# Kernel optimization log

Hardware: AMD Instinct MI355X
Metric: run time of the kernel (lower is better)

The kernel has to match this reference:

```python
import jax, jax.numpy as jnp
import numpy as np

N_TOKENS = 2048
HIDDEN = 2880
N_HEADS = 64          # total query heads
N_KV = 8              # key/value heads
Q_MULT = N_HEADS // N_KV
HEAD_DIM = 64
SLIDING_WINDOW = 128  # layer_idx=0 -> sliding-window layer
SM_SCALE = 1.0 / np.sqrt(HEAD_DIM)
RMS_EPS = 1e-5
ROPE_BASE = 150000.0
ROPE_SCALING = 32.0
INIT_CTX = 4096
NTK_ALPHA = 1.0
NTK_BETA = 32.0


def _rope_tables(num_tokens):
    # YaRN NTK-by-parts inverse frequencies (static constants)
    freq = ROPE_BASE ** (np.arange(0, HEAD_DIM, 2, dtype=np.float64) / HEAD_DIM)
    concentration = 0.1 * np.log(ROPE_SCALING) + 1.0
    d_half = HEAD_DIM / 2
    low = d_half * np.log(INIT_CTX / (NTK_BETA * 2 * np.pi)) / np.log(ROPE_BASE)
    high = d_half * np.log(INIT_CTX / (NTK_ALPHA * 2 * np.pi)) / np.log(ROPE_BASE)
    interpolation = 1.0 / (ROPE_SCALING * freq)
    extrapolation = 1.0 / freq
    ramp = (np.arange(d_half) - low) / (high - low)
    m = 1.0 - np.clip(ramp, 0.0, 1.0)
    inv_freq = interpolation * (1.0 - m) + extrapolation * m
    t = np.arange(num_tokens, dtype=np.float64)
    freqs = np.outer(t, inv_freq)
    cos = jnp.asarray((np.cos(freqs) * concentration), dtype=jnp.float32)
    sin = jnp.asarray((np.sin(freqs) * concentration), dtype=jnp.float32)
    return cos, sin  # [num_tokens, HEAD_DIM//2]


def _apply_rotary(x, cos, sin):
    # x: [n, heads, HEAD_DIM]
    c = cos[:, None, :].astype(x.dtype)
    s = sin[:, None, :].astype(x.dtype)
    x1, x2 = jnp.split(x, 2, axis=-1)
    return jnp.concatenate([x1 * c - x2 * s, x2 * c + x1 * s], axis=-1)


def setup_inputs() -> dict:
    key = jax.random.key(0)
    ks = jax.random.split(key, 7)
    return {
        "x": jax.random.normal(ks[0], (N_TOKENS, HIDDEN), jnp.float32),
        "scale": jax.random.uniform(ks[1], (HIDDEN,), jnp.float32, 0.5, 1.5),
        "sink": jax.random.normal(ks[2], (N_HEADS,), jnp.float32),
        "w_qkv": jax.random.normal(ks[3], (HIDDEN, (N_HEADS + 2 * N_KV) * HEAD_DIM), jnp.float32) * 0.02,
        "b_qkv": jax.random.normal(ks[4], ((N_HEADS + 2 * N_KV) * HEAD_DIM,), jnp.float32) * 0.02,
        "w_o": jax.random.normal(ks[5], (N_HEADS * HEAD_DIM, HIDDEN), jnp.float32) * 0.02,
        "b_o": jax.random.normal(ks[6], (HIDDEN,), jnp.float32) * 0.02,
    }


def reference(x, scale, sink, w_qkv, b_qkv, w_o, b_o):
    n = x.shape[0]
    # RMSNorm (fp32)
    t = x.astype(jnp.float32)
    rms = jnp.sqrt(jnp.mean(t * t, axis=-1, keepdims=True) + RMS_EPS)
    t = (t / rms) * scale

    # QKV projection + split
    qkv = t @ w_qkv + b_qkv
    q_sz = N_HEADS * HEAD_DIM
    kv_sz = N_KV * HEAD_DIM
    q = qkv[:, :q_sz].reshape(n, N_HEADS, HEAD_DIM)
    k = qkv[:, q_sz:q_sz + kv_sz].reshape(n, N_KV, HEAD_DIM)
    v = qkv[:, q_sz + kv_sz:].reshape(n, N_KV, HEAD_DIM)

    # RoPE (YaRN)
    cos, sin = _rope_tables(n)
    q = _apply_rotary(q, cos, sin)
    k = _apply_rotary(k, cos, sin)

    # GQA layout: [n, N_KV, Q_MULT, HEAD_DIM]
    qg = q.reshape(n, N_KV, Q_MULT, HEAD_DIM)

    # scores: [N_KV, Q_MULT, n_q, n_kv]
    scores = jnp.einsum('nhgd,mhd->hgnm', qg, k) * SM_SCALE

    # causal + sliding-window mask
    q_pos = jnp.arange(n)[:, None]
    kv_pos = jnp.arange(n)[None, :]
    mask = jnp.where(kv_pos > q_pos, -jnp.inf, 0.0)
    mask = mask + jnp.where((SLIDING_WINDOW > 0) & (q_pos - kv_pos > SLIDING_WINDOW), -jnp.inf, 0.0)
    scores = scores + mask[None, None, :, :].astype(scores.dtype)

    # sink logit appended as extra softmax column, then dropped
    s_col = jnp.broadcast_to(sink.reshape(N_KV, Q_MULT, 1, 1), (N_KV, Q_MULT, n, 1))
    w = jax.nn.softmax(jnp.concatenate([scores, s_col], axis=-1), axis=-1)[..., :-1]

    attn = jnp.einsum('hgnm,mhd->nhgd', w, v).reshape(n, N_HEADS * HEAD_DIM)
    out = attn @ w_o + b_o
    return x + out


if __name__ == '__main__':
    inp = setup_inputs()
    y = reference(**inp)
    print(y.shape, y.dtype)
```

## Files before the change

### kernel.cpp

```cpp
#include <hip/hip_runtime.h>
#include <cstdint>
#include <cstddef>

#define HIDDEN   2880
#define QKV_N    5120
#define OPROJ_K  4096
#define NTOK     2048
#define WIN      128
#define SM_SCALE 0.125f

typedef _Float16 half8  __attribute__((ext_vector_type(8)));
typedef _Float16 half4v __attribute__((ext_vector_type(4)));
typedef float    f32x4  __attribute__((ext_vector_type(4)));

__device__ __forceinline__ void gload16(const void* g, void* l) {
  __builtin_amdgcn_global_load_lds((__attribute__((address_space(1))) void*)g,
                                   (__attribute__((address_space(3))) void*)l,
                                   16, 0, 0);
}

__device__ __forceinline__ _Float16 f2h(float f) { return (_Float16)f; }

#define NB_CQ  (160 * 90)
#define NB_CO  (92 * 128)
#define NB_ROPE 256

__device__ __forceinline__ void cast_transpose_body(const float* __restrict__ W,
                                                    _Float16* __restrict__ Wt,
                                                    int K, int N, int n0, int k0,
                                                    float* tile ) {
  int t = threadIdx.x;
  #pragma unroll
  for (int p = 0; p < 4; ++p) {
    int e = t + p * 256; int r = e >> 5, cc = e & 31;
    float vv = 0.f;
    if (n0 + cc < N) vv = W[(size_t)(k0 + r) * N + n0 + cc];
    tile[r * 33 + cc] = vv;
  }
  __syncthreads();
  {
    int r = t >> 3, c4 = (t & 7) * 4;
    half4v h;
    #pragma unroll
    for (int u = 0; u < 4; ++u) h[u] = (_Float16)tile[(c4 + u) * 33 + r];
    *(half4v*)&Wt[(size_t)(n0 + r) * K + k0 + c4] = h;
  }
}

__global__ __launch_bounds__(256) void prep_kernel(const float* __restrict__ x,
                                                   const float* __restrict__ scale,
                                                   const float* __restrict__ w_qkv,
                                                   const float* __restrict__ w_o,
                                                   _Float16* __restrict__ a_h,
                                                   _Float16* __restrict__ wtq,
                                                   _Float16* __restrict__ wto,
                                                   float2* __restrict__ tab) {
  __shared__ float smem[32 * 33];
  int b = blockIdx.x, t = threadIdx.x;
  if (b < NB_CQ) {
    cast_transpose_body(w_qkv, wtq, HIDDEN, QKV_N, (b % 160) * 32, (b / 160) * 32, smem);
    return;
  }
  b -= NB_CQ;
  if (b < NB_CO) {
    cast_transpose_body(w_o, wto, OPROJ_K, HIDDEN, (b % 92) * 32, (b / 92) * 32, smem);
    return;
  }
  b -= NB_CO;
  if (b < NTOK) {
    int row = b;
    const float4* xr = (const float4*)(x + (size_t)row * HIDDEN);
    const float4* sc = (const float4*)scale;
    float4 v0 = xr[t];
    float4 v1 = xr[t + 256];
    float4 v2 = (t < 208) ? xr[t + 512] : make_float4(0.f, 0.f, 0.f, 0.f);
    float ss = v0.x*v0.x + v0.y*v0.y + v0.z*v0.z + v0.w*v0.w
             + v1.x*v1.x + v1.y*v1.y + v1.z*v1.z + v1.w*v1.w
             + v2.x*v2.x + v2.y*v2.y + v2.z*v2.z + v2.w*v2.w;
    #pragma unroll
    for (int m = 1; m < 64; m <<= 1) ss += __shfl_xor(ss, m, 64);
    if ((t & 63) == 0) smem[t >> 6] = ss;
    __syncthreads();
    float inv = 1.0f / sqrtf((smem[0] + smem[1] + smem[2] + smem[3]) * (1.0f / HIDDEN) + 1e-5f);
    _Float16* orow = a_h + (size_t)row * HIDDEN;
    auto store4 = [&](int c4, const float4& v, const float4& s) {
      half4v h;
      h[0] = f2h(v.x * inv * s.x); h[1] = f2h(v.y * inv * s.y);
      h[2] = f2h(v.z * inv * s.z); h[3] = f2h(v.w * inv * s.w);
      *(half4v*)(orow + (size_t)c4 * 4) = h;
    };
    store4(t, v0, sc[t]);
    store4(t + 256, v1, sc[t + 256]);
    if (t < 208) store4(t + 512, v2, sc[t + 512]);
    return;
  }
  b -= NTOK;
  {
    int idx = b * 256 + t;
    int tok = idx >> 5, d = idx & 31;
    const double PI = 3.14159265358979323846;
    double i = (double)d;
    double lf = log(150000.0);
    double freq = exp(lf * (i / 32.0));
    double interp = 1.0 / (32.0 * freq);
    double extrap = 1.0 / freq;
    double low  = 32.0 * log(4096.0 / (32.0 * 2.0 * PI)) / lf;
    double high = 32.0 * log(4096.0 / (2.0 * PI)) / lf;
    double ramp = (i - low) / (high - low);
    double mm = 1.0 - fmin(fmax(ramp, 0.0), 1.0);
    double invf = interp * (1.0 - mm) + extrap * mm;
    double ang = (double)tok * invf;
    double conc = 0.1 * log(32.0) + 1.0;
    tab[idx] = make_float2((float)(cos(ang) * conc), (float)(sin(ang) * conc));
  }
}

template <int BM, bool QKV_MODE>
__global__ __launch_bounds__(256, 2) void gemm_kernel(const _Float16* __restrict__ A,
                                                      const _Float16* __restrict__ Bt,
                                                      const float* __restrict__ bias,
                                                      const float* __restrict__ resid,
                                                      const float2* __restrict__ tab,
                                                      void* __restrict__ Cout,
                                                      int M, int N, int K) {
  constexpr int MI = BM / 32;
  constexpr int NA = BM / 32;
  __shared__ _Float16 Alds[BM * 64];
  __shared__ _Float16 Blds[128 * 64];
  int tid = threadIdx.x;
  int wave = tid >> 6, lane = tid & 63;
  int wm = wave >> 1, wn = wave & 1;
  int c = lane & 15, quad = lane >> 4;
  int m0 = blockIdx.y * BM, n0 = blockIdx.x * 128;

  const _Float16* gAp[NA]; _Float16* lAp[NA];
  #pragma unroll
  for (int i = 0; i < NA; ++i) {
    int p = wave * 64 + i * 256 + lane;
    int r = p >> 3;
    int kl = (p & 7) ^ (r & 7);
    gAp[i] = A + (size_t)(m0 + r) * K + kl * 8;
    lAp[i] = Alds + (size_t)(wave * 64 + i * 256) * 8;
  }
  const _Float16* gBp[4]; _Float16* lBp[4];
  #pragma unroll
  for (int i = 0; i < 4; ++i) {
    int p = wave * 64 + i * 256 + lane;
    int r = p >> 3;
    int kl = (p & 7) ^ (r & 7);
    gBp[i] = Bt + (size_t)(n0 + r) * K + kl * 8;
    lBp[i] = Blds + (size_t)(wave * 64 + i * 256) * 8;
  }

  int px[2];
  px[0] = ((0 * 4 + quad) ^ (c & 7)) * 8;
  px[1] = ((1 * 4 + quad) ^ (c & 7)) * 8;

  f32x4 acc[MI][4] = {};
  int nIter = K >> 6;
  for (int kt = 0; kt < nIter; ++kt) {
    __syncthreads();
    #pragma unroll
    for (int i = 0; i < NA; ++i) { gload16(gAp[i], lAp[i]); gAp[i] += 64; }
    #pragma unroll
    for (int i = 0; i < 4; ++i)  { gload16(gBp[i], lBp[i]); gBp[i] += 64; }
    __syncthreads();
    half8 a[MI][2], b[4][2];
    #pragma unroll
    for (int i = 0; i < MI; ++i) {
      int row = wm * (BM / 2) + i * 16 + c;
      a[i][0] = *(const half8*)&Alds[row * 64 + px[0]];
      a[i][1] = *(const half8*)&Alds[row * 64 + px[1]];
    }
    #pragma unroll
    for (int j = 0; j < 4; ++j) {
      int row = wn * 64 + j * 16 + c;
      b[j][0] = *(const half8*)&Blds[row * 64 + px[0]];
      b[j][1] = *(const half8*)&Blds[row * 64 + px[1]];
    }
    #pragma unroll
    for (int i = 0; i < MI; ++i)
      #pragma unroll
      for (int j = 0; j < 4; ++j) {
        acc[i][j] = __builtin_amdgcn_mfma_f32_16x16x32_f16(a[i][0], b[j][0], acc[i][j], 0, 0, 0);
        acc[i][j] = __builtin_amdgcn_mfma_f32_16x16x32_f16(a[i][1], b[j][1], acc[i][j], 0, 0, 0);
      }
  }

  if (QKV_MODE) {
    _Float16* outp = (_Float16*)Cout;
    bool ropeTile = (n0 < 4608);
    #pragma unroll
    for (int i = 0; i < MI; ++i) {
      int rowb = m0 + wm * (BM / 2) + i * 16 + quad * 4;
      if (ropeTile) {
        #pragma unroll
        for (int jp = 0; jp < 2; ++jp) {
          int col = n0 + wn * 64 + jp * 16 + c;
          float b1 = bias[col], b2 = bias[col + 32];
          #pragma unroll
          for (int r = 0; r < 4; ++r) {
            float2 cs = tab[(size_t)(rowb + r) * 32 + jp * 16 + c];
            float x1 = acc[i][jp][r] + b1;
            float x2 = acc[i][jp + 2][r] + b2;
            outp[(size_t)(rowb + r) * QKV_N + col]      = f2h(x1 * cs.x - x2 * cs.y);
            outp[(size_t)(rowb + r) * QKV_N + col + 32] = f2h(x2 * cs.x + x1 * cs.y);
          }
        }
      } else {
        #pragma unroll
        for (int j = 0; j < 4; ++j) {
          int col = n0 + wn * 64 + j * 16 + c;
          float bv = bias[col];
          #pragma unroll
          for (int r = 0; r < 4; ++r)
            outp[(size_t)(rowb + r) * QKV_N + col] = f2h(acc[i][j][r] + bv);
        }
      }
    }
  } else {
    float* outp = (float*)Cout;
    #pragma unroll
    for (int i = 0; i < MI; ++i) {
      int rowb = m0 + wm * (BM / 2) + i * 16 + quad * 4;
      #pragma unroll
      for (int j = 0; j < 4; ++j) {
        int col = n0 + wn * 64 + j * 16 + c;
        if (col < N) {
          float bv = bias[col];
          #pragma unroll
          for (int r = 0; r < 4; ++r)
            outp[(size_t)(rowb + r) * N + col] =
                acc[i][j][r] + bv + resid[(size_t)(rowb + r) * N + col];
        }
      }
    }
  }
}

#define TQ 16
__global__ __launch_bounds__(256) void attn_kernel(const _Float16* __restrict__ qkv,
                                                   const float* __restrict__ sink,
                                                   _Float16* __restrict__ attn_out) {
  __shared__ _Float16 Vt[64 * 160];
  __shared__ _Float16 Ps[128 * 160];
  int qt = blockIdx.x, kvh = blockIdx.y;
  int Q0 = qt * TQ;
  int kmin = (Q0 >= WIN) ? Q0 - WIN : 0;
  int nkv = Q0 + TQ - kmin;
  int tid = threadIdx.x;
  int wave = tid >> 6, lane = tid & 63;
  int c = lane & 15, quad = lane >> 4;

  #pragma unroll
  for (int p = 0; p < 5; ++p) {
    int cc = p * 256 + tid;
    int col = cc % 160;
    int d0 = (cc / 160) * 8;
    union { uint4 u4; _Float16 hv[8]; } buf;
    if (col < nkv) buf.u4 = *(const uint4*)(qkv + (size_t)(kmin + col) * QKV_N + 4608 + kvh * 64 + d0);
    else           buf.u4 = make_uint4(0, 0, 0, 0);
    #pragma unroll
    for (int uu = 0; uu < 8; ++uu) Vt[(d0 + uu) * 160 + col] = buf.hv[uu];
  }
  #pragma unroll
  for (int p = 0; p < 8; ++p) {
    int idx = p * 256 + tid;
    Ps[(idx >> 4) * 160 + 144 + (idx & 15)] = (_Float16)0.f;
  }

  half8 aq[2][2];
  #pragma unroll
  for (int i = 0; i < 2; ++i) {
    int qm = wave * 2 + i;
    #pragma unroll
    for (int ks = 0; ks < 2; ++ks)
      aq[i][ks] = *(const half8*)(qkv + (size_t)(Q0 + c) * QKV_N + (kvh * 8 + qm) * 64 + ks * 32 + quad * 8);
  }

  f32x4 sacc[2][9] = {};
  #pragma unroll
  for (int j = 0; j < 9; ++j) {
    #pragma unroll
    for (int ks = 0; ks < 2; ++ks) {
      half8 bk = *(const half8*)(qkv + (size_t)(kmin + j * 16 + c) * QKV_N + 4096 + kvh * 64 + ks * 32 + quad * 8);
      #pragma unroll
      for (int i = 0; i < 2; ++i)
        sacc[i][j] = __builtin_amdgcn_mfma_f32_16x16x32_f16(aq[i][ks], bk, sacc[i][j], 0, 0, 0);
    }
  }

  #pragma unroll
  for (int i = 0; i < 2; ++i) {
    int qm = wave * 2 + i;
    float sk = sink[kvh * 8 + qm];
    #pragma unroll
    for (int r = 0; r < 4; ++r) {
      int qpos = Q0 + quad * 4 + r;
      float sv[9]; float mx = -3e38f;
      #pragma unroll
      for (int j = 0; j < 9; ++j) {
        int key = kmin + j * 16 + c;
        float s = sacc[i][j][r] * SM_SCALE;
        bool valid = (key <= qpos) && (qpos - key <= WIN);
        sv[j] = valid ? s : -3e38f;
        mx = fmaxf(mx, sv[j]);
      }
      #pragma unroll
      for (int msk = 1; msk < 16; msk <<= 1) mx = fmaxf(mx, __shfl_xor(mx, msk, 64));
      mx = fmaxf(mx, sk);
      float sum = 0.f; float pv[9];
      #pragma unroll
      for (int j = 0; j < 9; ++j) { float p = __expf(sv[j] - mx); pv[j] = p; sum += p; }
      #pragma unroll
      for (int msk = 1; msk < 16; msk <<= 1) sum += __shfl_xor(sum, msk, 64);
      sum += __expf(sk - mx);
      float inv = 1.0f / sum;
      int mrow = qm * 16 + quad * 4 + r;
      #pragma unroll
      for (int j = 0; j < 9; ++j)
        Ps[mrow * 160 + j * 16 + c] = f2h(pv[j] * inv);
    }
  }

  __syncthreads();

  f32x4 oacc[2][4] = {};
  #pragma unroll
  for (int ks = 0; ks < 5; ++ks) {
    half8 ap[2], bv[4];
    #pragma unroll
    for (int i = 0; i < 2; ++i)
      ap[i] = *(const half8*)&Ps[((wave * 2 + i) * 16 + c) * 160 + ks * 32 + quad * 8];
    #pragma unroll
    for (int j = 0; j < 4; ++j)
      bv[j] = *(const half8*)&Vt[(j * 16 + c) * 160 + ks * 32 + quad * 8];
    #pragma unroll
    for (int i = 0; i < 2; ++i)
      #pragma unroll
      for (int j = 0; j < 4; ++j)
        oacc[i][j] = __builtin_amdgcn_mfma_f32_16x16x32_f16(ap[i], bv[j], oacc[i][j], 0, 0, 0);
  }

  #pragma unroll
  for (int i = 0; i < 2; ++i) {
    int qm = wave * 2 + i;
    #pragma unroll
    for (int j = 0; j < 4; ++j)
      #pragma unroll
      for (int r = 0; r < 4; ++r) {
        int token = Q0 + quad * 4 + r;
        attn_out[(size_t)token * 4096 + (kvh * 8 + qm) * 64 + j * 16 + c] = f2h(oacc[i][j][r]);
      }
  }
}

extern "C" void kernel_launch(void* const* d_in, const int* in_sizes, int n_in,
                              void* d_out, int out_size, void* d_ws, size_t ws_size,
                              hipStream_t stream) {
  (void)in_sizes; (void)n_in; (void)out_size; (void)ws_size;
  const float* x      = (const float*)d_in[0];
  const float* scale  = (const float*)d_in[1];
  const float* sink   = (const float*)d_in[2];
  const float* w_qkv  = (const float*)d_in[3];
  const float* b_qkv  = (const float*)d_in[4];
  const float* w_o    = (const float*)d_in[5];
  const float* b_o    = (const float*)d_in[6];
  float* out = (float*)d_out;

  char* ws = (char*)d_ws;
  size_t off = 0;
  auto alloc = [&](size_t bytes) { void* p = ws + off; off += (bytes + 255) & ~(size_t)255; return p; };
  float2*   tab   = (float2*)alloc((size_t)NTOK * 32 * sizeof(float2));
  _Float16* a_h   = (_Float16*)alloc((size_t)NTOK * HIDDEN * 2);
  _Float16* wtq   = (_Float16*)alloc((size_t)QKV_N * HIDDEN * 2);
  _Float16* wto   = (_Float16*)alloc((size_t)2944 * OPROJ_K * 2);
  _Float16* qkv_h = (_Float16*)alloc((size_t)NTOK * QKV_N * 2);
  _Float16* at_h  = (_Float16*)alloc((size_t)NTOK * 4096 * 2);

  int prep_blocks = NB_CQ + NB_CO + NTOK + NB_ROPE;
  prep_kernel<<<prep_blocks, 256, 0, stream>>>(x, scale, w_qkv, w_o, a_h, wtq, wto, tab);
  gemm_kernel<128, true><<<dim3(QKV_N / 128, NTOK / 128), 256, 0, stream>>>(
      a_h, wtq, b_qkv, nullptr, tab, qkv_h, NTOK, QKV_N, HIDDEN);
  attn_kernel<<<dim3(NTOK / TQ, 8), 256, 0, stream>>>(qkv_h, sink, at_h);
  gemm_kernel<64, false><<<dim3(23, NTOK / 64), 256, 0, stream>>>(
      at_h, wto, b_o, x, nullptr, out, NTOK, HIDDEN, OPROJ_K);
}
```

Before: 343.6 us.

## Widen weight transpose tiles, stage Q/K in LDS, tune GEMM occupancy, reuse workspace

The weight cast-transpose now uses 64x64 tiles with 16-byte half8 stores, so fewer blocks are launched and stores are wider. The attention kernel stages K and Q tiles into swizzled LDS through async global-to-LDS loads instead of strided global loads per MFMA, and aliases the score buffer over the same shared memory. GEMM launch bounds now request 3 or 4 waves per SIMD, which may constrain registers and cause spills. The attention output buffer reuses the QKV weight workspace to shrink the memory footprint.

Measured after the change: 336.4 us. 1.02x faster.

```diff
diff --git a/kernel.cpp b/kernel.cpp
--- a/kernel.cpp
+++ b/kernel.cpp
@@ -21,29 +21,31 @@
 
 __device__ __forceinline__ _Float16 f2h(float f) { return (_Float16)f; }
 
-#define NB_CQ  (160 * 90)
-#define NB_CO  (92 * 128)
+#define NB_T0  (80 * 45)
+#define NB_T1  (46 * 64)
 #define NB_ROPE 256
 
-__device__ __forceinline__ void cast_transpose_body(const float* __restrict__ W,
-                                                    _Float16* __restrict__ Wt,
-                                                    int K, int N, int n0, int k0,
-                                                    float* tile ) {
+__device__ __forceinline__ void cast_transpose64(const float* __restrict__ W,
+                                                 _Float16* __restrict__ Wt,
+                                                 int K, int N, int n0, int k0,
+                                                 float* tile ) {
   int t = threadIdx.x;
   #pragma unroll
-  for (int p = 0; p < 4; ++p) {
-    int e = t + p * 256; int r = e >> 5, cc = e & 31;
+  for (int p = 0; p < 16; ++p) {
+    int r = p * 4 + (t >> 6), cc = t & 63;
     float vv = 0.f;
     if (n0 + cc < N) vv = W[(size_t)(k0 + r) * N + n0 + cc];
-    tile[r * 33 + cc] = vv;
+    tile[r * 65 + cc] = vv;
   }
   __syncthreads();
-  {
-    int r = t >> 3, c4 = (t & 7) * 4;
-    half4v h;
-    #pragma unroll
-    for (int u = 0; u < 4; ++u) h[u] = (_Float16)tile[(c4 + u) * 33 + r];
-    *(half4v*)&Wt[(size_t)(n0 + r) * K + k0 + c4] = h;
+  #pragma unroll
+  for (int p = 0; p < 2; ++p) {
+    int idx = p * 256 + t;
+    int r = idx >> 3, ch = (idx & 7) * 8;
+    half8 h;
+    #pragma unroll
+    for (int u = 0; u < 8; ++u) h[u] = (_Float16)tile[(ch + u) * 65 + r];
+    *(half8*)&Wt[(size_t)(n0 + r) * K + k0 + ch] = h;
   }
 }
 
@@ -55,18 +57,18 @@
                                                    _Float16* __restrict__ wtq,
                                                    _Float16* __restrict__ wto,
                                                    float2* __restrict__ tab) {
-  __shared__ float smem[32 * 33];
+  __shared__ float smem[64 * 65];
   int b = blockIdx.x, t = threadIdx.x;
-  if (b < NB_CQ) {
-    cast_transpose_body(w_qkv, wtq, HIDDEN, QKV_N, (b % 160) * 32, (b / 160) * 32, smem);
+  if (b < NB_T0) {
+    cast_transpose64(w_qkv, wtq, HIDDEN, QKV_N, (b % 80) * 64, (b / 80) * 64, smem);
     return;
   }
-  b -= NB_CQ;
-  if (b < NB_CO) {
-    cast_transpose_body(w_o, wto, OPROJ_K, HIDDEN, (b % 92) * 32, (b / 92) * 32, smem);
+  b -= NB_T0;
+  if (b < NB_T1) {
+    cast_transpose64(w_o, wto, OPROJ_K, HIDDEN, (b % 46) * 64, (b / 46) * 64, smem);
     return;
   }
-  b -= NB_CO;
+  b -= NB_T1;
   if (b < NTOK) {
     int row = b;
     const float4* xr = (const float4*)(x + (size_t)row * HIDDEN);
@@ -115,14 +117,14 @@
   }
 }
 
-template <int BM, bool QKV_MODE>
-__global__ __launch_bounds__(256, 2) void gemm_kernel(const _Float16* __restrict__ A,
-                                                      const _Float16* __restrict__ Bt,
-                                                      const float* __restrict__ bias,
-                                                      const float* __restrict__ resid,
-                                                      const float2* __restrict__ tab,
-                                                      void* __restrict__ Cout,
-                                                      int M, int N, int K) {
+template <int BM, bool QKV_MODE, int MINW>
+__global__ __launch_bounds__(256, MINW) void gemm_kernel(const _Float16* __restrict__ A,
+                                                         const _Float16* __restrict__ Bt,
+                                                         const float* __restrict__ bias,
+                                                         const float* __restrict__ resid,
+                                                         const float2* __restrict__ tab,
+                                                         void* __restrict__ Cout,
+                                                         int M, int N, int K) {
   constexpr int MI = BM / 32;
   constexpr int NA = BM / 32;
   __shared__ _Float16 Alds[BM * 64];
@@ -242,8 +244,12 @@
 __global__ __launch_bounds__(256) void attn_kernel(const _Float16* __restrict__ qkv,
                                                    const float* __restrict__ sink,
                                                    _Float16* __restrict__ attn_out) {
-  __shared__ _Float16 Vt[64 * 160];
-  __shared__ _Float16 Ps[128 * 160];
+  __shared__ __align__(16) char smem[61440];
+  _Float16* Klds = (_Float16*)smem;
+  _Float16* Qlds = (_Float16*)(smem + 20480);
+  _Float16* Ps   = (_Float16*)smem;
+  _Float16* Vt   = (_Float16*)(smem + 40960);
+
   int qt = blockIdx.x, kvh = blockIdx.y;
   int Q0 = qt * TQ;
   int kmin = (Q0 >= WIN) ? Q0 - WIN : 0;
@@ -252,6 +258,28 @@
   int wave = tid >> 6, lane = tid & 63;
   int c = lane & 15, quad = lane >> 4;
 
+  {
+    const _Float16* kbase = qkv + 4096 + kvh * 64;
+    #pragma unroll
+    for (int p = 0; p < 5; ++p) {
+      int ci = p * 256 + wave * 64 + lane;
+      int row = ci >> 3, pc = ci & 7;
+      int lc = pc ^ (row & 7);
+      gload16(kbase + (size_t)(kmin + row) * QKV_N + lc * 8,
+              (char*)Klds + (size_t)(p * 256 + wave * 64) * 16);
+    }
+  }
+  {
+    const _Float16* qbase = qkv + kvh * 512;
+    #pragma unroll
+    for (int p = 0; p < 4; ++p) {
+      int ci = p * 256 + wave * 64 + lane;
+      int tok = ci >> 6, Lp = ci & 63;
+      int Llog = (Lp & 56) | ((Lp ^ tok) & 7);
+      gload16(qbase + (size_t)(Q0 + tok) * QKV_N + Llog * 8,
+              (char*)Qlds + (size_t)(p * 256 + wave * 64) * 16);
+    }
+  }
   #pragma unroll
   for (int p = 0; p < 5; ++p) {
     int cc = p * 256 + tid;
@@ -263,31 +291,41 @@
     #pragma unroll
     for (int uu = 0; uu < 8; ++uu) Vt[(d0 + uu) * 160 + col] = buf.hv[uu];
   }
+
+  __syncthreads();
+
+  half8 aq[2][2];
+  #pragma unroll
+  for (int i = 0; i < 2; ++i) {
+    int qm = wave * 2 + i;
+    #pragma unroll
+    for (int ks = 0; ks < 2; ++ks) {
+      int kc = ks * 4 + quad;
+      int Lp = qm * 8 + (kc ^ (c & 7));
+      aq[i][ks] = *(const half8*)&Qlds[c * 512 + Lp * 8];
+    }
+  }
+
+  f32x4 sacc[2][9] = {};
+  #pragma unroll
+  for (int j = 0; j < 9; ++j) {
+    #pragma unroll
+    for (int ks = 0; ks < 2; ++ks) {
+      int kc = ks * 4 + quad;
+      int pc = kc ^ (c & 7);
+      half8 bk = *(const half8*)&Klds[(j * 16 + c) * 64 + pc * 8];
+      #pragma unroll
+      for (int i = 0; i < 2; ++i)
+        sacc[i][j] = __builtin_amdgcn_mfma_f32_16x16x32_f16(aq[i][ks], bk, sacc[i][j], 0, 0, 0);
+    }
+  }
+
+  __syncthreads();
+
   #pragma unroll
   for (int p = 0; p < 8; ++p) {
     int idx = p * 256 + tid;
     Ps[(idx >> 4) * 160 + 144 + (idx & 15)] = (_Float16)0.f;
-  }
-
-  half8 aq[2][2];
-  #pragma unroll
-  for (int i = 0; i < 2; ++i) {
-    int qm = wave * 2 + i;
-    #pragma unroll
-    for (int ks = 0; ks < 2; ++ks)
-      aq[i][ks] = *(const half8*)(qkv + (size_t)(Q0 + c) * QKV_N + (kvh * 8 + qm) * 64 + ks * 32 + quad * 8);
-  }
-
-  f32x4 sacc[2][9] = {};
-  #pragma unroll
-  for (int j = 0; j < 9; ++j) {
-    #pragma unroll
-    for (int ks = 0; ks < 2; ++ks) {
-      half8 bk = *(const half8*)(qkv + (size_t)(kmin + j * 16 + c) * QKV_N + 4096 + kvh * 64 + ks * 32 + quad * 8);
-      #pragma unroll
-      for (int i = 0; i < 2; ++i)
-        sacc[i][j] = __builtin_amdgcn_mfma_f32_16x16x32_f16(aq[i][ks], bk, sacc[i][j], 0, 0, 0);
-    }
   }
 
   #pragma unroll
@@ -371,18 +409,18 @@
   char* ws = (char*)d_ws;
   size_t off = 0;
   auto alloc = [&](size_t bytes) { void* p = ws + off; off += (bytes + 255) & ~(size_t)255; return p; };
-  float2*   tab   = (float2*)alloc((size_t)NTOK * 32 * sizeof(float2));
-  _Float16* a_h   = (_Float16*)alloc((size_t)NTOK * HIDDEN * 2);
   _Float16* wtq   = (_Float16*)alloc((size_t)QKV_N * HIDDEN * 2);
   _Float16* wto   = (_Float16*)alloc((size_t)2944 * OPROJ_K * 2);
+  _Float16* a_h   = (_Float16*)alloc((size_t)NTOK * HIDDEN * 2);
   _Float16* qkv_h = (_Float16*)alloc((size_t)NTOK * QKV_N * 2);
-  _Float16* at_h  = (_Float16*)alloc((size_t)NTOK * 4096 * 2);
-
-  int prep_blocks = NB_CQ + NB_CO + NTOK + NB_ROPE;
+  float2*   tab   = (float2*)alloc((size_t)NTOK * 32 * sizeof(float2));
+  _Float16* at_h  = (_Float16*)wtq;
+
+  int prep_blocks = NB_T0 + NB_T1 + NTOK + NB_ROPE;
   prep_kernel<<<prep_blocks, 256, 0, stream>>>(x, scale, w_qkv, w_o, a_h, wtq, wto, tab);
-  gemm_kernel<128, true><<<dim3(QKV_N / 128, NTOK / 128), 256, 0, stream>>>(
+  gemm_kernel<128, true, 3><<<dim3(QKV_N / 128, NTOK / 128), 256, 0, stream>>>(
       a_h, wtq, b_qkv, nullptr, tab, qkv_h, NTOK, QKV_N, HIDDEN);
   attn_kernel<<<dim3(NTOK / TQ, 8), 256, 0, stream>>>(qkv_h, sink, at_h);
-  gemm_kernel<64, false><<<dim3(23, NTOK / 64), 256, 0, stream>>>(
+  gemm_kernel<64, false, 4><<<dim3(23, NTOK / 64), 256, 0, stream>>>(
       at_h, wto, b_o, x, nullptr, out, NTOK, HIDDEN, OPROJ_K);
 }
```
